# Optimization experiments

Hardware: AMD Instinct MI355X
Metric: run time of the kernel (lower is better)

The kernel has to match this reference:

```python
import jax, jax.numpy as jnp
import numpy as np

EPS = 1e-10

def _feature_map(x):
    # fm(None) defaults to elu(x) + 1 (canonical linear-attention feature map)
    return jax.nn.elu(x) + 1.0

def setup_inputs() -> dict:
    key = jax.random.key(0)
    k1, k2, k3 = jax.random.split(key, 3)
    N, L, H, D = 4, 8192, 16, 64
    return {
        "queries": jax.random.normal(k1, (N, L, H, D), dtype=jnp.float32),
        "keys": jax.random.normal(k2, (N, L, H, D), dtype=jnp.float32),
        "values": jax.random.normal(k3, (N, L, H, D), dtype=jnp.float32),
    }

def reference(queries, keys, values):
    Q = _feature_map(queries)  # [n,l,h,d]
    K = _feature_map(keys)     # [n,s,h,d]
    # KV reduction over sequence: [n,h,m,d]
    KV = jnp.einsum('nshd,nshm->nhmd', K, values)
    # Normalizer: 1 / (Q . sum_s K) + eps (eps added AFTER reciprocal, as in source)
    Z = 1.0 / jnp.einsum('nlhd,nhd->nlh', Q, K.sum(axis=1)) + EPS
    # Output: [n,l,h,m]
    out = jnp.einsum('nlhd,nhmd,nlh->nlhm', Q, KV, Z)
    return out
```

## Files before the change

kernel.cpp:

```cpp
#include <hip/hip_runtime.h>


#define EPSV      1e-10f
#define L_SEQ     8192
#define NH_TOT    64
#define ROWSTRIDE 1024
#define KV_STRIDE 4160
#define SLICE     (NH_TOT * KV_STRIDE)
#define QSTRIDE   68

__device__ __forceinline__ float fm(float x) {
    return x > 0.0f ? x + 1.0f : __expf(x);
}

__global__ __launch_bounds__(256) void kv_reduce_kernel(
    const float* __restrict__ K, const float* __restrict__ V,
    float* __restrict__ ws, int tiles, int mode)
{
    const int t     = threadIdx.x;
    const int nh    = blockIdx.x;
    const int chunk = blockIdx.y;
    const int n  = nh >> 4, h = nh & 15;

    const int rg = t >> 4;
    const int dq = (t & 15) << 2;
    const int d0 = (t >> 4) << 2;
    const int m0 = (t & 15) << 2;

    __shared__ float Kl[32 * 64];
    __shared__ float Vl[32 * 64];

    float acc[4][4] = {};
    float ks[4] = {0.f, 0.f, 0.f, 0.f};

    const int base = n * (L_SEQ * ROWSTRIDE) + h * 64;
    const int s0   = chunk * (tiles * 32);

    float4 kr0, kr1, vr0, vr1;
    {
        const int ga0 = base + (s0 + rg) * ROWSTRIDE + dq;
        const int ga1 = ga0 + 16 * ROWSTRIDE;
        kr0 = *reinterpret_cast<const float4*>(K + ga0);
        kr1 = *reinterpret_cast<const float4*>(K + ga1);
        vr0 = *reinterpret_cast<const float4*>(V + ga0);
        vr1 = *reinterpret_cast<const float4*>(V + ga1);
    }

    for (int tile = 0; tile < tiles; ++tile) {
        float4 kf0, kf1;
        kf0.x = fm(kr0.x); kf0.y = fm(kr0.y); kf0.z = fm(kr0.z); kf0.w = fm(kr0.w);
        kf1.x = fm(kr1.x); kf1.y = fm(kr1.y); kf1.z = fm(kr1.z); kf1.w = fm(kr1.w);
        ks[0] += kf0.x + kf1.x; ks[1] += kf0.y + kf1.y;
        ks[2] += kf0.z + kf1.z; ks[3] += kf0.w + kf1.w;
        *reinterpret_cast<float4*>(&Kl[rg * 64 + dq])        = kf0;
        *reinterpret_cast<float4*>(&Kl[(rg + 16) * 64 + dq]) = kf1;
        *reinterpret_cast<float4*>(&Vl[rg * 64 + dq])        = vr0;
        *reinterpret_cast<float4*>(&Vl[(rg + 16) * 64 + dq]) = vr1;
        __syncthreads();

        if (tile + 1 < tiles) {
            const int ga0 = base + (s0 + (tile + 1) * 32 + rg) * ROWSTRIDE + dq;
            const int ga1 = ga0 + 16 * ROWSTRIDE;
            kr0 = *reinterpret_cast<const float4*>(K + ga0);
            kr1 = *reinterpret_cast<const float4*>(K + ga1);
            vr0 = *reinterpret_cast<const float4*>(V + ga0);
            vr1 = *reinterpret_cast<const float4*>(V + ga1);
        }

#pragma unroll 8
        for (int s = 0; s < 32; ++s) {
            const float4 k4 = *reinterpret_cast<const float4*>(&Kl[s * 64 + d0]);
            const float4 v4 = *reinterpret_cast<const float4*>(&Vl[s * 64 + m0]);
            acc[0][0] += k4.x * v4.x; acc[0][1] += k4.x * v4.y; acc[0][2] += k4.x * v4.z; acc[0][3] += k4.x * v4.w;
            acc[1][0] += k4.y * v4.x; acc[1][1] += k4.y * v4.y; acc[1][2] += k4.y * v4.z; acc[1][3] += k4.y * v4.w;
            acc[2][0] += k4.z * v4.x; acc[2][1] += k4.z * v4.y; acc[2][2] += k4.z * v4.z; acc[2][3] += k4.z * v4.w;
            acc[3][0] += k4.w * v4.x; acc[3][1] += k4.w * v4.y; acc[3][2] += k4.w * v4.z; acc[3][3] += k4.w * v4.w;
        }
        __syncthreads();
    }

    float* ksp = Vl;
    *reinterpret_cast<float4*>(&ksp[rg * 64 + dq]) = *reinterpret_cast<float4*>(ks);
    __syncthreads();

    float* dst = ws + (size_t)(mode ? (chunk * NH_TOT + nh) : nh) * KV_STRIDE;

    if (mode) {
#pragma unroll
        for (int i = 0; i < 4; ++i) {
            float4 o; o.x = acc[i][0]; o.y = acc[i][1]; o.z = acc[i][2]; o.w = acc[i][3];
            *reinterpret_cast<float4*>(dst + (d0 + i) * 64 + m0) = o;
        }
        if (t < 64) {
            float ssum = 0.f;
#pragma unroll
            for (int g = 0; g < 16; ++g) ssum += ksp[g * 64 + t];
            dst[4096 + t] = ssum;
        }
    } else {
#pragma unroll
        for (int i = 0; i < 4; ++i)
#pragma unroll
            for (int j = 0; j < 4; ++j)
                atomicAdd(dst + (d0 + i) * 64 + (m0 + j), acc[i][j]);
        if (t < 64) {
            float ssum = 0.f;
#pragma unroll
            for (int g = 0; g < 16; ++g) ssum += ksp[g * 64 + t];
            atomicAdd(dst + 4096 + t, ssum);
        }
    }
}

__global__ __launch_bounds__(256) void reduce_kernel(float* __restrict__ ws, int CH)
{
    const int idx = blockIdx.x * 256 + threadIdx.x;
    float s = 0.f;
    for (int c = 0; c < CH; ++c) s += ws[(size_t)c * SLICE + idx];
    ws[idx] = s;
}

__global__ __launch_bounds__(256) void out_kernel(
    const float* __restrict__ Q, const float* __restrict__ KVg,
    float* __restrict__ out)
{
    const int t      = threadIdx.x;
    const int lchunk = blockIdx.x;
    const int nh     = blockIdx.y;
    const int n = nh >> 4, h = nh & 15;

    __shared__ float Ql[64 * QSTRIDE];
    __shared__ float KVl[4096];
    __shared__ float Ks[64];
    __shared__ float zl[64];

    const float* kvrow = KVg + (size_t)nh * KV_STRIDE;

#pragma unroll
    for (int j = 0; j < 4; ++j) {
        reinterpret_cast<float4*>(KVl)[t + 256 * j] =
            reinterpret_cast<const float4*>(kvrow)[t + 256 * j];
    }
    if (t < 16) {
        reinterpret_cast<float4*>(Ks)[t] =
            reinterpret_cast<const float4*>(kvrow + 4096)[t];
    }
    __syncthreads();

    const int lane16 = t & 15, grp = t >> 4;
    const int dq = lane16 << 2;
    const float4 ks4 = *reinterpret_cast<const float4*>(&Ks[dq]);
    const int qbase = (n * L_SEQ + lchunk * 64) * ROWSTRIDE + h * 64;
#pragma unroll
    for (int p = 0; p < 4; ++p) {
        const int rr = p * 16 + grp;
        const float4 qg = *reinterpret_cast<const float4*>(Q + qbase + rr * ROWSTRIDE + dq);
        float4 qf;
        qf.x = fm(qg.x); qf.y = fm(qg.y); qf.z = fm(qg.z); qf.w = fm(qg.w);
        *reinterpret_cast<float4*>(&Ql[rr * QSTRIDE + dq]) = qf;
        float dp = qf.x * ks4.x + qf.y * ks4.y + qf.z * ks4.z + qf.w * ks4.w;
        dp += __shfl_xor(dp, 1);
        dp += __shfl_xor(dp, 2);
        dp += __shfl_xor(dp, 4);
        dp += __shfl_xor(dp, 8);
        if (lane16 == 0) zl[rr] = 1.0f / dp + EPSV;
    }
    __syncthreads();

    const int r0 = grp << 2;
    const int c0 = lane16 << 2;
    float acc[4][4] = {};
#pragma unroll 2
    for (int d = 0; d < 64; d += 4) {
        const float4 b0 = *reinterpret_cast<const float4*>(&KVl[(d + 0) * 64 + c0]);
        const float4 b1 = *reinterpret_cast<const float4*>(&KVl[(d + 1) * 64 + c0]);
        const float4 b2 = *reinterpret_cast<const float4*>(&KVl[(d + 2) * 64 + c0]);
        const float4 b3 = *reinterpret_cast<const float4*>(&KVl[(d + 3) * 64 + c0]);
#define DO_ROW(i) do {                                                              \
        const float4 q = *reinterpret_cast<const float4*>(&Ql[(r0 + (i)) * QSTRIDE + d]); \
        acc[i][0] += q.x * b0.x + q.y * b1.x + q.z * b2.x + q.w * b3.x;             \
        acc[i][1] += q.x * b0.y + q.y * b1.y + q.z * b2.y + q.w * b3.y;             \
        acc[i][2] += q.x * b0.z + q.y * b1.z + q.z * b2.z + q.w * b3.z;             \
        acc[i][3] += q.x * b0.w + q.y * b1.w + q.z * b2.w + q.w * b3.w;             \
    } while (0)
        DO_ROW(0); DO_ROW(1); DO_ROW(2); DO_ROW(3);
#undef DO_ROW
    }

    const int obase = qbase;
#pragma unroll
    for (int i = 0; i < 4; ++i) {
        const float z = zl[r0 + i];
        float4 o;
        o.x = acc[i][0] * z; o.y = acc[i][1] * z; o.z = acc[i][2] * z; o.w = acc[i][3] * z;
        *reinterpret_cast<float4*>(out + obase + (r0 + i) * ROWSTRIDE + c0) = o;
    }
}

extern "C" void kernel_launch(void* const* d_in, const int* in_sizes, int n_in,
                              void* d_out, int out_size, void* d_ws, size_t ws_size,
                              hipStream_t stream) {
    const float* Q = (const float*)d_in[0];
    const float* K = (const float*)d_in[1];
    const float* V = (const float*)d_in[2];
    float* out = (float*)d_out;
    float* ws  = (float*)d_ws;

    const size_t per_slice = (size_t)SLICE * sizeof(float);
    size_t max_ch = ws_size / per_slice;
    int CH = max_ch >= 32 ? 32 : (max_ch >= 16 ? 16 : (max_ch >= 8 ? 8 : 0));

    if (CH > 0) {
        const int tiles = (L_SEQ / 32) / CH;
        kv_reduce_kernel<<<dim3(NH_TOT, CH), 256, 0, stream>>>(K, V, ws, tiles, 1);
        reduce_kernel<<<SLICE / 256, 256, 0, stream>>>(ws, CH);
    } else {
        hipMemsetAsync(d_ws, 0, per_slice, stream);
        kv_reduce_kernel<<<dim3(NH_TOT, 16), 256, 0, stream>>>(K, V, ws, 16, 0);
    }
    out_kernel<<<dim3(L_SEQ / 64, NH_TOT), 256, 0, stream>>>(Q, ws, out);
}
```

Baseline: 187.3 us.

## Compute KV outer products per wave via shuffles and hoist out_kernel loads

The KV reduction kernel drops the LDS tiles and per-tile block barriers. Each wave now owns its own slice of rows and broadcasts K and V values with __shfl into an 8x8 register tile per lane. Partial results from the four waves are combined through LDS at the end, and the chunk count falls from 32 to 16. In the output kernel, all KV and Q global loads are issued up front to raise memory-level parallelism. The tradeoff is heavy shuffle traffic and a 64-float accumulator per lane, which adds register pressure under the launch bound of (256, 4).

```diff
diff --git a/kernel.cpp b/kernel.cpp
--- a/kernel.cpp
+++ b/kernel.cpp
@@ -13,102 +13,118 @@
     return x > 0.0f ? x + 1.0f : __expf(x);
 }
 
-__global__ __launch_bounds__(256) void kv_reduce_kernel(
+__global__ __launch_bounds__(256, 4) void kv_reduce_kernel(
     const float* __restrict__ K, const float* __restrict__ V,
-    float* __restrict__ ws, int tiles, int mode)
+    float* __restrict__ ws, int rows_per_wave, int mode)
 {
-    const int t     = threadIdx.x;
-    const int nh    = blockIdx.x;
-    const int chunk = blockIdx.y;
-    const int n  = nh >> 4, h = nh & 15;
-
-    const int rg = t >> 4;
-    const int dq = (t & 15) << 2;
-    const int d0 = (t >> 4) << 2;
-    const int m0 = (t & 15) << 2;
-
-    __shared__ float Kl[32 * 64];
-    __shared__ float Vl[32 * 64];
-
-    float acc[4][4] = {};
-    float ks[4] = {0.f, 0.f, 0.f, 0.f};
-
-    const int base = n * (L_SEQ * ROWSTRIDE) + h * 64;
-    const int s0   = chunk * (tiles * 32);
-
-    float4 kr0, kr1, vr0, vr1;
-    {
-        const int ga0 = base + (s0 + rg) * ROWSTRIDE + dq;
-        const int ga1 = ga0 + 16 * ROWSTRIDE;
-        kr0 = *reinterpret_cast<const float4*>(K + ga0);
-        kr1 = *reinterpret_cast<const float4*>(K + ga1);
-        vr0 = *reinterpret_cast<const float4*>(V + ga0);
-        vr1 = *reinterpret_cast<const float4*>(V + ga1);
-    }
-
-    for (int tile = 0; tile < tiles; ++tile) {
-        float4 kf0, kf1;
-        kf0.x = fm(kr0.x); kf0.y = fm(kr0.y); kf0.z = fm(kr0.z); kf0.w = fm(kr0.w);
-        kf1.x = fm(kr1.x); kf1.y = fm(kr1.y); kf1.z = fm(kr1.z); kf1.w = fm(kr1.w);
-        ks[0] += kf0.x + kf1.x; ks[1] += kf0.y + kf1.y;
-        ks[2] += kf0.z + kf1.z; ks[3] += kf0.w + kf1.w;
-        *reinterpret_cast<float4*>(&Kl[rg * 64 + dq])        = kf0;
-        *reinterpret_cast<float4*>(&Kl[(rg + 16) * 64 + dq]) = kf1;
-        *reinterpret_cast<float4*>(&Vl[rg * 64 + dq])        = vr0;
-        *reinterpret_cast<float4*>(&Vl[(rg + 16) * 64 + dq]) = vr1;
-        __syncthreads();
-
-        if (tile + 1 < tiles) {
-            const int ga0 = base + (s0 + (tile + 1) * 32 + rg) * ROWSTRIDE + dq;
-            const int ga1 = ga0 + 16 * ROWSTRIDE;
-            kr0 = *reinterpret_cast<const float4*>(K + ga0);
-            kr1 = *reinterpret_cast<const float4*>(K + ga1);
-            vr0 = *reinterpret_cast<const float4*>(V + ga0);
-            vr1 = *reinterpret_cast<const float4*>(V + ga1);
+    const int t    = threadIdx.x;
+    const int nh   = blockIdx.x;
+    const int chunk= blockIdx.y;
+    const int n = nh >> 4, h = nh & 15;
+    const int wid  = t >> 6;
+    const int lane = t & 63;
+
+    const int d0 = (lane >> 3) << 3;
+    const int m0 = (lane & 7) << 3;
+    const int kb = d0 >> 2;
+    const int mb = m0 >> 2;
+
+    const int rp = lane >> 4;
+    const int qd = (lane & 15) << 2;
+
+    float acc[8][8] = {};
+    float ks0 = 0.f, ks1 = 0.f, ks2 = 0.f, ks3 = 0.f;
+
+    const size_t base  = (size_t)n * (L_SEQ * ROWSTRIDE) + h * 64;
+    const int    srow0 = chunk * (rows_per_wave * 4) + wid * rows_per_wave;
+    const float* Kp = K + base + (size_t)srow0 * ROWSTRIDE;
+    const float* Vp = V + base + (size_t)srow0 * ROWSTRIDE;
+    const size_t lofs = (size_t)rp * ROWSTRIDE + qd;
+
+    const int ngroups = rows_per_wave >> 2;
+
+    float4 kg = *reinterpret_cast<const float4*>(Kp + lofs);
+    float4 vg = *reinterpret_cast<const float4*>(Vp + lofs);
+
+    for (int g = 0; g < ngroups; ++g) {
+        float4 kf, vv = vg;
+        kf.x = fm(kg.x); kf.y = fm(kg.y); kf.z = fm(kg.z); kf.w = fm(kg.w);
+        ks0 += kf.x; ks1 += kf.y; ks2 += kf.z; ks3 += kf.w;
+
+        if (g + 1 < ngroups) {
+            const size_t o = (size_t)(g + 1) * (4 * ROWSTRIDE) + lofs;
+            kg = *reinterpret_cast<const float4*>(Kp + o);
+            vg = *reinterpret_cast<const float4*>(Vp + o);
         }
 
-#pragma unroll 8
-        for (int s = 0; s < 32; ++s) {
-            const float4 k4 = *reinterpret_cast<const float4*>(&Kl[s * 64 + d0]);
-            const float4 v4 = *reinterpret_cast<const float4*>(&Vl[s * 64 + m0]);
-            acc[0][0] += k4.x * v4.x; acc[0][1] += k4.x * v4.y; acc[0][2] += k4.x * v4.z; acc[0][3] += k4.x * v4.w;
-            acc[1][0] += k4.y * v4.x; acc[1][1] += k4.y * v4.y; acc[1][2] += k4.y * v4.z; acc[1][3] += k4.y * v4.w;
-            acc[2][0] += k4.z * v4.x; acc[2][1] += k4.z * v4.y; acc[2][2] += k4.z * v4.z; acc[2][3] += k4.z * v4.w;
-            acc[3][0] += k4.w * v4.x; acc[3][1] += k4.w * v4.y; acc[3][2] += k4.w * v4.z; acc[3][3] += k4.w * v4.w;
+#pragma unroll
+        for (int r = 0; r < 4; ++r) {
+            const int sk = (r << 4) + kb;
+            const int sv = (r << 4) + mb;
+            float ka[8], va[8];
+            ka[0] = __shfl(kf.x, sk);     ka[1] = __shfl(kf.y, sk);
+            ka[2] = __shfl(kf.z, sk);     ka[3] = __shfl(kf.w, sk);
+            ka[4] = __shfl(kf.x, sk + 1); ka[5] = __shfl(kf.y, sk + 1);
+            ka[6] = __shfl(kf.z, sk + 1); ka[7] = __shfl(kf.w, sk + 1);
+            va[0] = __shfl(vv.x, sv);     va[1] = __shfl(vv.y, sv);
+            va[2] = __shfl(vv.z, sv);     va[3] = __shfl(vv.w, sv);
+            va[4] = __shfl(vv.x, sv + 1); va[5] = __shfl(vv.y, sv + 1);
+            va[6] = __shfl(vv.z, sv + 1); va[7] = __shfl(vv.w, sv + 1);
+#pragma unroll
+            for (int j = 0; j < 8; ++j)
+#pragma unroll
+                for (int q = 0; q < 8; ++q)
+                    acc[j][q] += ka[j] * va[q];
+        }
+    }
+
+    ks0 += __shfl_xor(ks0, 16); ks0 += __shfl_xor(ks0, 32);
+    ks1 += __shfl_xor(ks1, 16); ks1 += __shfl_xor(ks1, 32);
+    ks2 += __shfl_xor(ks2, 16); ks2 += __shfl_xor(ks2, 32);
+    ks3 += __shfl_xor(ks3, 16); ks3 += __shfl_xor(ks3, 32);
+
+    __shared__ float red[4096];
+    __shared__ float ksred[256];
+    if (lane < 16) {
+        reinterpret_cast<float4*>(ksred)[wid * 16 + lane] =
+            make_float4(ks0, ks1, ks2, ks3);
+    }
+
+    for (int w = 0; w < 4; ++w) {
+        if (wid == w) {
+#pragma unroll
+            for (int j = 0; j < 8; ++j) {
+                float* p = &red[(d0 + j) * 64 + m0];
+                float4 a0 = make_float4(acc[j][0], acc[j][1], acc[j][2], acc[j][3]);
+                float4 a1 = make_float4(acc[j][4], acc[j][5], acc[j][6], acc[j][7]);
+                if (w != 0) {
+                    float4 b0 = *reinterpret_cast<float4*>(p);
+                    float4 b1 = *reinterpret_cast<float4*>(p + 4);
+                    a0.x += b0.x; a0.y += b0.y; a0.z += b0.z; a0.w += b0.w;
+                    a1.x += b1.x; a1.y += b1.y; a1.z += b1.z; a1.w += b1.w;
+                }
+                *reinterpret_cast<float4*>(p)     = a0;
+                *reinterpret_cast<float4*>(p + 4) = a1;
+            }
         }
         __syncthreads();
     }
 
-    float* ksp = Vl;
-    *reinterpret_cast<float4*>(&ksp[rg * 64 + dq]) = *reinterpret_cast<float4*>(ks);
-    __syncthreads();
-
     float* dst = ws + (size_t)(mode ? (chunk * NH_TOT + nh) : nh) * KV_STRIDE;
-
     if (mode) {
 #pragma unroll
-        for (int i = 0; i < 4; ++i) {
-            float4 o; o.x = acc[i][0]; o.y = acc[i][1]; o.z = acc[i][2]; o.w = acc[i][3];
-            *reinterpret_cast<float4*>(dst + (d0 + i) * 64 + m0) = o;
-        }
-        if (t < 64) {
-            float ssum = 0.f;
-#pragma unroll
-            for (int g = 0; g < 16; ++g) ssum += ksp[g * 64 + t];
-            dst[4096 + t] = ssum;
-        }
+        for (int i = 0; i < 4; ++i)
+            *reinterpret_cast<float4*>(dst + t * 16 + i * 4) =
+                *reinterpret_cast<const float4*>(&red[t * 16 + i * 4]);
+        if (t < 64)
+            dst[4096 + t] = ksred[t] + ksred[64 + t] + ksred[128 + t] + ksred[192 + t];
     } else {
 #pragma unroll
-        for (int i = 0; i < 4; ++i)
-#pragma unroll
-            for (int j = 0; j < 4; ++j)
-                atomicAdd(dst + (d0 + i) * 64 + (m0 + j), acc[i][j]);
-        if (t < 64) {
-            float ssum = 0.f;
-#pragma unroll
-            for (int g = 0; g < 16; ++g) ssum += ksp[g * 64 + t];
-            atomicAdd(dst + 4096 + t, ssum);
-        }
+        for (int i = 0; i < 16; ++i)
+            atomicAdd(dst + t * 16 + i, red[t * 16 + i]);
+        if (t < 64)
+            atomicAdd(dst + 4096 + t,
+                      ksred[t] + ksred[64 + t] + ksred[128 + t] + ksred[192 + t]);
     }
 }
 
@@ -131,30 +147,32 @@
 
     __shared__ float Ql[64 * QSTRIDE];
     __shared__ float KVl[4096];
-    __shared__ float Ks[64];
     __shared__ float zl[64];
 
     const float* kvrow = KVg + (size_t)nh * KV_STRIDE;
-
-#pragma unroll
-    for (int j = 0; j < 4; ++j) {
-        reinterpret_cast<float4*>(KVl)[t + 256 * j] =
-            reinterpret_cast<const float4*>(kvrow)[t + 256 * j];
-    }
-    if (t < 16) {
-        reinterpret_cast<float4*>(Ks)[t] =
-            reinterpret_cast<const float4*>(kvrow + 4096)[t];
-    }
-    __syncthreads();
-
     const int lane16 = t & 15, grp = t >> 4;
     const int dq = lane16 << 2;
-    const float4 ks4 = *reinterpret_cast<const float4*>(&Ks[dq]);
-    const int qbase = (n * L_SEQ + lchunk * 64) * ROWSTRIDE + h * 64;
+    const size_t qbase = ((size_t)n * L_SEQ + lchunk * 64) * ROWSTRIDE + h * 64;
+
+    const float4 kv0 = reinterpret_cast<const float4*>(kvrow)[t];
+    const float4 kv1 = reinterpret_cast<const float4*>(kvrow)[t + 256];
+    const float4 kv2 = reinterpret_cast<const float4*>(kvrow)[t + 512];
+    const float4 kv3 = reinterpret_cast<const float4*>(kvrow)[t + 768];
+    const float4 qg0 = *reinterpret_cast<const float4*>(Q + qbase + (size_t)(grp)      * ROWSTRIDE + dq);
+    const float4 qg1 = *reinterpret_cast<const float4*>(Q + qbase + (size_t)(16 + grp) * ROWSTRIDE + dq);
+    const float4 qg2 = *reinterpret_cast<const float4*>(Q + qbase + (size_t)(32 + grp) * ROWSTRIDE + dq);
+    const float4 qg3 = *reinterpret_cast<const float4*>(Q + qbase + (size_t)(48 + grp) * ROWSTRIDE + dq);
+    const float4 ks4 = *reinterpret_cast<const float4*>(kvrow + 4096 + dq);
+
+    reinterpret_cast<float4*>(KVl)[t]       = kv0;
+    reinterpret_cast<float4*>(KVl)[t + 256] = kv1;
+    reinterpret_cast<float4*>(KVl)[t + 512] = kv2;
+    reinterpret_cast<float4*>(KVl)[t + 768] = kv3;
+
 #pragma unroll
     for (int p = 0; p < 4; ++p) {
+        const float4 qg = (p == 0) ? qg0 : (p == 1) ? qg1 : (p == 2) ? qg2 : qg3;
         const int rr = p * 16 + grp;
-        const float4 qg = *reinterpret_cast<const float4*>(Q + qbase + rr * ROWSTRIDE + dq);
         float4 qf;
         qf.x = fm(qg.x); qf.y = fm(qg.y); qf.z = fm(qg.z); qf.w = fm(qg.w);
         *reinterpret_cast<float4*>(&Ql[rr * QSTRIDE + dq]) = qf;
@@ -187,13 +205,12 @@
 #undef DO_ROW
     }
 
-    const int obase = qbase;
 #pragma unroll
     for (int i = 0; i < 4; ++i) {
         const float z = zl[r0 + i];
         float4 o;
         o.x = acc[i][0] * z; o.y = acc[i][1] * z; o.z = acc[i][2] * z; o.w = acc[i][3] * z;
-        *reinterpret_cast<float4*>(out + obase + (r0 + i) * ROWSTRIDE + c0) = o;
+        *reinterpret_cast<float4*>(out + qbase + (size_t)(r0 + i) * ROWSTRIDE + c0) = o;
     }
 }
 
@@ -208,15 +225,15 @@
 
     const size_t per_slice = (size_t)SLICE * sizeof(float);
     size_t max_ch = ws_size / per_slice;
-    int CH = max_ch >= 32 ? 32 : (max_ch >= 16 ? 16 : (max_ch >= 8 ? 8 : 0));
+    int CH = max_ch >= 16 ? 16 : (max_ch >= 8 ? 8 : 0);
 
     if (CH > 0) {
-        const int tiles = (L_SEQ / 32) / CH;
-        kv_reduce_kernel<<<dim3(NH_TOT, CH), 256, 0, stream>>>(K, V, ws, tiles, 1);
+        const int rows_per_wave = L_SEQ / (CH * 4);
+        kv_reduce_kernel<<<dim3(NH_TOT, CH), 256, 0, stream>>>(K, V, ws, rows_per_wave, 1);
         reduce_kernel<<<SLICE / 256, 256, 0, stream>>>(ws, CH);
     } else {
         hipMemsetAsync(d_ws, 0, per_slice, stream);
-        kv_reduce_kernel<<<dim3(NH_TOT, 16), 256, 0, stream>>>(K, V, ws, 16, 0);
+        kv_reduce_kernel<<<dim3(NH_TOT, 16), 256, 0, stream>>>(K, V, ws, L_SEQ / 64, 0);
     }
     out_kernel<<<dim3(L_SEQ / 64, NH_TOT), 256, 0, stream>>>(Q, ws, out);
 }
```

Measured after the change: 202.8 us. +8.3%, slower.
